# Kernel tuning notes

Hardware: AMD Instinct MI355X
Metric: run time of the kernel (lower is better)

Reference implementation:

```python
import jax, jax.numpy as jnp
import numpy as np

C1 = 512  # channels1 (query input dim)
C = 512   # channels (model dim)


def setup_inputs() -> dict:
    key = jax.random.key(0)
    ks = jax.random.split(key, 12)
    B, Lq, Lk = 8, 2048, 2048
    s1 = 1.0 / np.sqrt(C1)
    s = 1.0 / np.sqrt(C)
    return {
        "rep": jax.random.normal(ks[0], (B, Lq, C1), dtype=jnp.float32),
        "rep1": jax.random.normal(ks[1], (B, Lk, C), dtype=jnp.float32),
        "Wq_w": jax.random.uniform(ks[2], (C1, C), jnp.float32, -s1, s1),
        "Wq_b": jax.random.uniform(ks[3], (C,), jnp.float32, -s1, s1),
        "Wk_w": jax.random.uniform(ks[4], (C, C), jnp.float32, -s, s),
        "Wk_b": jax.random.uniform(ks[5], (C,), jnp.float32, -s, s),
        "Wv_w": jax.random.uniform(ks[6], (C, C), jnp.float32, -s, s),
        "Wv_b": jax.random.uniform(ks[7], (C,), jnp.float32, -s, s),
        "FC_w": jax.random.uniform(ks[8], (C, C), jnp.float32, -s, s),
        "FC_b": jax.random.uniform(ks[9], (C,), jnp.float32, -s, s),
    }


def reference(rep, rep1, Wq_w, Wq_b, Wk_w, Wk_b, Wv_w, Wv_b, FC_w, FC_b):
    # Linear + ReLU projections (single head)
    q = jax.nn.relu(jnp.einsum('blc,cd->bld', rep, Wq_w) + Wq_b)    # [B,Lq,C]
    k = jax.nn.relu(jnp.einsum('blc,cd->bld', rep1, Wk_w) + Wk_b)   # [B,Lk,C]
    v = jax.nn.relu(jnp.einsum('blc,cd->bld', rep1, Wv_w) + Wv_b)   # [B,Lk,C]
    scores = jnp.einsum('bqd,bkd->bqk', q, k) / jnp.sqrt(jnp.float32(C))
    attn = jax.nn.softmax(scores, axis=-1)                           # [B,Lq,Lk]
    out = jnp.einsum('bqk,bkd->bqd', attn, v)                        # [B,Lq,C]
    out = jax.nn.relu(jnp.einsum('bld,de->ble', out, FC_w) + FC_b)
    return out
```

## Files before the change

### kernel.cpp

```cpp
#include <hip/hip_runtime.h>


typedef __attribute__((ext_vector_type(8))) short short8;
typedef __attribute__((ext_vector_type(4))) float f32x4;

#define SEQ 2048
#define CH 512
#define NB 8
#define MTOT (NB * SEQ)

#define GLDS16(gp, lp)                                                                  \
  __builtin_amdgcn_global_load_lds((const __attribute__((address_space(1))) void*)(gp), \
                                   (__attribute__((address_space(3))) void*)(lp), 16, 0, 0)

__device__ __forceinline__ unsigned short f2bf(float f) {
  unsigned u = __float_as_uint(f);
  u += 0x7fffu + ((u >> 16) & 1u);
  return (unsigned short)(u >> 16);
}

__device__ __forceinline__ unsigned pack2bf(float lo, float hi) {
  return __builtin_amdgcn_perm(__float_as_uint(hi), __float_as_uint(lo), 0x07060302u);
}

__global__ __launch_bounds__(256) void prep2_kernel(
    const float* __restrict__ W0, const float* __restrict__ W1,
    const float* __restrict__ W2, const float* __restrict__ W3,
    unsigned short* __restrict__ Wt,
    const float* __restrict__ Wk_b, const float* __restrict__ Wv_b,
    float* __restrict__ biasKV, float* __restrict__ rowsum) {
  __shared__ __attribute__((aligned(16))) unsigned short tile[64 * 72];
  const int blk = blockIdx.x;
  const int t = threadIdx.x;
  if (blk < 256) {
    const int z = blk >> 6;
    const int bx = blk & 7, by = (blk >> 3) & 7;
    const float* W = (z == 0) ? W0 : (z == 1) ? W1 : (z == 2) ? W2 : W3;
    unsigned short* Wtz = Wt + (long)z * 512 * 512;
    const int k0 = by * 64, n0 = bx * 64;
    const int r = t >> 4, cq = (t & 15) * 4;
#pragma unroll
    for (int j = 0; j < 4; ++j) {
      int row = r + 16 * j;
      float4 v = *(const float4*)&W[(long)(k0 + row) * 512 + n0 + cq];
      tile[row * 72 + cq + 0] = f2bf(v.x);
      tile[row * 72 + cq + 1] = f2bf(v.y);
      tile[row * 72 + cq + 2] = f2bf(v.z);
      tile[row * 72 + cq + 3] = f2bf(v.w);
    }
    __syncthreads();
#pragma unroll
    for (int j = 0; j < 4; ++j) {
      int row = r + 16 * j;
      ushort4 o;
      o.x = tile[(cq + 0) * 72 + row];
      o.y = tile[(cq + 1) * 72 + row];
      o.z = tile[(cq + 2) * 72 + row];
      o.w = tile[(cq + 3) * 72 + row];
      *(ushort4*)&Wtz[(long)(n0 + row) * 512 + k0 + cq] = o;
    }
  } else if (blk == 256) {
    biasKV[t] = Wk_b[t];
    biasKV[t + 256] = Wk_b[t + 256];
    biasKV[t + 512] = Wv_b[t];
    biasKV[t + 768] = Wv_b[t + 256];
  } else {
    const int zb = blk - 257;
    f32x4 z4 = {0.f, 0.f, 0.f, 0.f};
    *(f32x4*)&rowsum[(zb * 256 + t) * 4] = z4;
  }
}

template <int LDO>
__device__ __forceinline__ void proj_body(const float* __restrict__ A,
                                          const unsigned short* __restrict__ Bt,
                                          const float* __restrict__ bias,
                                          unsigned short* __restrict__ Op,
                                          long m0, long n0, unsigned short* smem) {
  float* Af = (float*)smem;
  unsigned short* Bl = smem + 8192;
  const int t = threadIdx.x;
  const int w = t >> 6, l = t & 63;
  const int wr = w >> 1, wc = w & 1;
  const int lr = l & 15, lg = l >> 4;
  const float* ga = A + (m0 + 32 * w + (l >> 3)) * CH + ((l & 7) ^ (l >> 3)) * 4;
  const unsigned short* gb =
      Bt + (n0 + 32 * w + (l >> 2)) * CH + (((l & 3) ^ ((l >> 3) & 3)) * 8);
  float* la = Af + 32 * w * 32;
  unsigned short* lb = Bl + 32 * w * 32;

  f32x4 acc[4][4] = {};
  for (int k0 = 0; k0 < CH; k0 += 32) {
#pragma unroll
    for (int j = 0; j < 4; ++j) GLDS16(ga + 8 * j * CH, la + 8 * j * 32);
    GLDS16(gb, lb);
    GLDS16(gb + 16 * CH, lb + 16 * 32);
    ga += 32; gb += 32;
    __syncthreads();
    short8 af[4], bfr[4];
#pragma unroll
    for (int i = 0; i < 4; ++i) {
      const int row = 64 * wr + 16 * i + lr;
      f32x4 a0 = *(f32x4*)&Af[row * 32 + ((2 * lg) ^ (lr & 7)) * 4];
      f32x4 a1 = *(f32x4*)&Af[row * 32 + ((2 * lg + 1) ^ (lr & 7)) * 4];
      union { unsigned u[4]; short8 s; } pk;
      pk.u[0] = pack2bf(a0[0], a0[1]);
      pk.u[1] = pack2bf(a0[2], a0[3]);
      pk.u[2] = pack2bf(a1[0], a1[1]);
      pk.u[3] = pack2bf(a1[2], a1[3]);
      af[i] = pk.s;
      bfr[i] = *(short8*)&Bl[(64 * wc + 16 * i + lr) * 32 + (lg ^ ((lr >> 1) & 3)) * 8];
    }
#pragma unroll
    for (int mi = 0; mi < 4; ++mi)
#pragma unroll
      for (int ni = 0; ni < 4; ++ni)
        acc[mi][ni] =
            __builtin_amdgcn_mfma_f32_16x16x32_bf16(af[mi], bfr[ni], acc[mi][ni], 0, 0, 0);
    __syncthreads();
  }
  unsigned short* patch = smem;
  float bv[4];
#pragma unroll
  for (int ni = 0; ni < 4; ++ni) bv[ni] = bias[n0 + 64 * wc + 16 * ni + lr];
#pragma unroll
  for (int mi = 0; mi < 4; ++mi)
#pragma unroll
    for (int ni = 0; ni < 4; ++ni)
#pragma unroll
      for (int r = 0; r < 4; ++r) {
        const int m = 64 * wr + 16 * mi + 4 * lg + r;
        const int n = 64 * wc + 16 * ni + lr;
        patch[m * 128 + ((n >> 3) ^ (m & 15)) * 8 + (n & 7)] =
            f2bf(fmaxf(acc[mi][ni][r] + bv[ni], 0.0f));
      }
  __syncthreads();
  const int q = t & 3;
#pragma unroll
  for (int p = 0; p < 2; ++p) {
    const int m = 64 * p + (t >> 2);
#pragma unroll
    for (int i = 0; i < 4; ++i) {
      const int cc = i * 4 + q;
      short8 x = *(short8*)&patch[m * 128 + ((cc ^ (m & 15)) * 8)];
      *(short8*)&Op[(m0 + m) * LDO + n0 + cc * 8] = x;
    }
  }
}

__global__ __launch_bounds__(256) void proj_kernel(const float* __restrict__ rep,
                                                   const float* __restrict__ rep1,
                                                   const unsigned short* __restrict__ Wt,
                                                   const float* __restrict__ Wq_b,
                                                   const float* __restrict__ biasKV,
                                                   unsigned short* __restrict__ Qb,
                                                   unsigned short* __restrict__ KVb) {
  __shared__ __attribute__((aligned(16))) unsigned short smem[16384];
  const long m0 = (long)blockIdx.y * 128;
  if (blockIdx.x < 4)
    proj_body<CH>(rep, Wt, Wq_b, Qb, m0, (long)blockIdx.x * 128, smem);
  else
    proj_body<1024>(rep1, Wt + 512 * 512, biasKV, KVb, m0, (long)(blockIdx.x - 4) * 128, smem);
}

template <int EPI, int LDA, int LDB, int LDO, int K, int BK>
__device__ __forceinline__ void gemm_body(const unsigned short* __restrict__ A,
                                          const unsigned short* __restrict__ Bt,
                                          const float* __restrict__ bias,
                                          float* __restrict__ rowsum,
                                          void* __restrict__ outp,
                                          long m0, long n0, unsigned short* smem) {
  unsigned short* Al = smem;
  unsigned short* Bl = smem + 128 * BK;
  const int t = threadIdx.x;
  const int w = t >> 6, l = t & 63;
  const int wr = w >> 1, wc = w & 1;
  const int lr = l & 15, lg = l >> 4;
  constexpr int NC = BK / 8;
  const int rl = l / NC, cc0 = l % NC;
  unsigned short* la = &Al[32 * w * BK];
  unsigned short* lb = &Bl[32 * w * BK];
  const int srow = 32 * w + rl;
  const int sxor = (cc0 ^ (rl & (NC - 1))) * 8;
  const unsigned short* ga = A + (m0 + srow) * (long)LDA + sxor;
  const unsigned short* gb = Bt + (n0 + srow) * (long)LDB + sxor;

  f32x4 acc[4][4] = {};
  for (int k0 = 0; k0 < K; k0 += BK) {
#pragma unroll
    for (int j = 0; j < 4; ++j) {
      GLDS16(ga + (long)8 * j * LDA, la + j * 8 * BK);
      GLDS16(gb + (long)8 * j * LDB, lb + j * 8 * BK);
    }
    ga += BK; gb += BK;
    __syncthreads();
#pragma unroll
    for (int h = 0; h < BK / 32; ++h) {
      short8 af[4], bfr[4];
#pragma unroll
      for (int i = 0; i < 4; ++i) {
        const int kc = ((h * 4 + lg) ^ (lr & (NC - 1))) * 8;
        af[i]  = *(short8*)&Al[(64 * wr + 16 * i + lr) * BK + kc];
        bfr[i] = *(short8*)&Bl[(64 * wc + 16 * i + lr) * BK + kc];
      }
#pragma unroll
      for (int mi = 0; mi < 4; ++mi)
#pragma unroll
        for (int ni = 0; ni < 4; ++ni)
          acc[mi][ni] =
              __builtin_amdgcn_mfma_f32_16x16x32_bf16(af[mi], bfr[ni], acc[mi][ni], 0, 0, 0);
    }
    __syncthreads();
  }

  unsigned short* patch = smem;
  float rsum[4][4] = {};
#pragma unroll
  for (int mi = 0; mi < 4; ++mi)
#pragma unroll
    for (int ni = 0; ni < 4; ++ni)
#pragma unroll
      for (int r = 0; r < 4; ++r) {
        const int m = 64 * wr + 16 * mi + 4 * lg + r;
        const int n = 64 * wc + 16 * ni + lr;
        float a = acc[mi][ni][r];
        unsigned short ob;
        if (EPI == 6) ob = f2bf(a);
        else {
          float p = exp2f(a * 0.06375872f);
          ob = f2bf(p);
          rsum[mi][r] += __uint_as_float((unsigned)ob << 16);
        }
        patch[m * 128 + ((n >> 3) ^ (m & 15)) * 8 + (n & 7)] = ob;
      }
  __syncthreads();
  unsigned short* O = (unsigned short*)outp;
  const int q = t & 3;
#pragma unroll
  for (int p = 0; p < 2; ++p) {
    const int m = 64 * p + (t >> 2);
#pragma unroll
    for (int i = 0; i < 4; ++i) {
      const int cc = i * 4 + q;
      short8 x = *(short8*)&patch[m * 128 + ((cc ^ (m & 15)) * 8)];
      *(short8*)&O[(m0 + m) * LDO + n0 + cc * 8] = x;
    }
  }
  if (EPI == 2) {
#pragma unroll
    for (int off = 1; off < 16; off <<= 1)
#pragma unroll
      for (int mi = 0; mi < 4; ++mi)
#pragma unroll
        for (int r = 0; r < 4; ++r) rsum[mi][r] += __shfl_xor(rsum[mi][r], off);
    if (lr == 0) {
#pragma unroll
      for (int mi = 0; mi < 4; ++mi)
#pragma unroll
        for (int r = 0; r < 4; ++r)
          atomicAdd(&rowsum[m0 + 64 * wr + 16 * mi + 4 * lg + r], rsum[mi][r]);
    }
  }
}

__global__ __launch_bounds__(256) void qkvf_kernel(const unsigned short* __restrict__ Qb,
                                                   const unsigned short* __restrict__ KVb,
                                                   const unsigned short* __restrict__ WtF,
                                                   float* __restrict__ rowsum,
                                                   unsigned short* __restrict__ Pbuf,
                                                   unsigned short* __restrict__ VFt) {
  __shared__ __attribute__((aligned(16))) unsigned short smem[2 * 128 * 64];
  const int bz = blockIdx.z;
  if (blockIdx.y < 16) {
    gemm_body<2, CH, 1024, SEQ, CH, 64>(
        Qb + (long)bz * SEQ * CH, KVb + (long)bz * SEQ * 1024, nullptr,
        rowsum + (long)bz * SEQ, Pbuf + (long)bz * SEQ * SEQ,
        (long)blockIdx.y * 128, (long)blockIdx.x * 128, smem);
  } else {
    gemm_body<6, CH, 1024, SEQ, CH, 64>(
        WtF, KVb + 512 + (long)bz * SEQ * 1024, nullptr, nullptr,
        VFt + (long)bz * CH * SEQ,
        (long)(blockIdx.y - 16) * 128, (long)blockIdx.x * 128, smem);
  }
}

#define CFENCE asm volatile("" ::: "memory")
#define SB0 __builtin_amdgcn_sched_barrier(0)
#define BAR8                          \
  do {                                \
    CFENCE;                           \
    __builtin_amdgcn_s_barrier();     \
    SB0;                              \
  } while (0)
#define LGKM0                                            \
  do {                                                   \
    asm volatile("s_waitcnt lgkmcnt(0)" ::: "memory");   \
    SB0;                                                 \
  } while (0)
#define VMC(n)                                              \
  do {                                                      \
    asm volatile("s_waitcnt vmcnt(" #n ")" ::: "memory");   \
    SB0;                                                    \
  } while (0)

__global__ __launch_bounds__(512, 2) void pvf_kernel(const unsigned short* __restrict__ Pbuf,
                                                     const unsigned short* __restrict__ VFt,
                                                     const float* __restrict__ FC_b,
                                                     float* __restrict__ rowsum,
                                                     float* __restrict__ out) {
  __shared__ __attribute__((aligned(16))) unsigned short smem[3][24576];
  const int s = blockIdx.x;
  const int xcd = s & 7, j = s >> 3;
  const int x = j & 3, pg = j >> 2;
  const int y = xcd, bz = pg;
  const long m0 = (long)y * 256, n0 = (long)x * 128;

  const unsigned short* A  = Pbuf + (long)bz * SEQ * SEQ;
  const unsigned short* Bt = VFt + (long)bz * CH * SEQ;
  constexpr int LDA = SEQ, LDB = SEQ;
  constexpr int NT = SEQ / 64;

  const int t = threadIdx.x;
  const int w = t >> 6, l = t & 63;
  const int wr = w >> 1, wc = w & 1;
  const int lr = l & 15, lg = l >> 4;

  const int srow = t >> 3;
  const int schk = ((t & 7) ^ ((t >> 3) & 7)) * 8;
  const unsigned short* gA = A + (m0 + srow) * (long)LDA + schk;
  const unsigned short* gB = Bt + (n0 + srow) * (long)LDB + schk;

  auto stageA = [&](int c, int kt) {
#pragma unroll
    for (int jj = 0; jj < 4; ++jj) {
      unsigned short* d = &smem[c][(64 * jj + 8 * w) * 64];
      GLDS16(gA + (long)(64 * jj) * LDA + (long)kt * 64, d);
    }
  };
  auto stageB = [&](int c, int kt) {
#pragma unroll
    for (int jj = 0; jj < 2; ++jj) {
      unsigned short* d = &smem[c][16384 + (64 * jj + 8 * w) * 64];
      GLDS16(gB + (long)(64 * jj) * LDB + (long)kt * 64, d);
    }
  };

  const int kx0 = (lg ^ (lr & 7)) * 8;
  const int kx1 = ((4 + lg) ^ (lr & 7)) * 8;
  short8 af[8], bf0[4], bf1[4];
  f32x4 acc[4][4] = {};

  auto readA = [&](int c) {
#pragma unroll
    for (int i = 0; i < 4; ++i) {
      const unsigned short* p = &smem[c][(64 * wr + 16 * i + lr) * 64];
      af[2 * i]     = *(const short8*)&p[kx0];
      af[2 * i + 1] = *(const short8*)&p[kx1];
    }
  };
  auto readB = [&](int c, int nh, short8* bf) {
#pragma unroll
    for (int i = 0; i < 2; ++i) {
      const unsigned short* p = &smem[c][16384 + (64 * wc + 16 * (2 * nh + i) + lr) * 64];
      bf[2 * i]     = *(const short8*)&p[kx0];
      bf[2 * i + 1] = *(const short8*)&p[kx1];
    }
  };
  auto quad = [&](int nh, const short8* bf) {
    __builtin_amdgcn_s_setprio(1);
#pragma unroll
    for (int mi = 0; mi < 4; ++mi)
#pragma unroll
      for (int jj = 0; jj < 2; ++jj) {
        acc[mi][2 * nh + jj] = __builtin_amdgcn_mfma_f32_16x16x32_bf16(
            af[2 * mi], bf[2 * jj], acc[mi][2 * nh + jj], 0, 0, 0);
        acc[mi][2 * nh + jj] = __builtin_amdgcn_mfma_f32_16x16x32_bf16(
            af[2 * mi + 1], bf[2 * jj + 1], acc[mi][2 * nh + jj], 0, 0, 0);
      }
    __builtin_amdgcn_s_setprio(0);
  };

  stageA(0, 0); stageB(0, 0);
  stageA(1, 1); stageB(1, 1);
  VMC(6);
  BAR8;

#pragma unroll
  for (int kt = 0; kt < NT; ++kt) {
    const int b = kt % 3, nb = (kt + 2) % 3;
    const bool st = (kt + 2) < NT;
    readA(b); readB(b, 0, bf0);
    if (st) stageA(nb, kt + 2);
    BAR8; LGKM0; quad(0, bf0); BAR8;
    readB(b, 1, bf1);
    if (st) { stageB(nb, kt + 2); VMC(6); } else { VMC(0); }
    BAR8; LGKM0; quad(1, bf1); BAR8;
  }

  __syncthreads();
  float* patchF = (float*)&smem[0][0];
  float bv[4];
#pragma unroll
  for (int ni = 0; ni < 4; ++ni) bv[ni] = FC_b[n0 + 64 * wc + 16 * ni + lr];
  float inv[4][4];
#pragma unroll
  for (int mi = 0; mi < 4; ++mi)
#pragma unroll
    for (int r = 0; r < 4; ++r)
      inv[mi][r] = 1.0f / rowsum[(long)bz * SEQ + m0 + 64 * wr + 16 * mi + 4 * lg + r];
#pragma unroll
  for (int mi = 0; mi < 4; ++mi)
#pragma unroll
    for (int ni = 0; ni < 4; ++ni)
#pragma unroll
      for (int r = 0; r < 4; ++r) {
        const int m = 64 * wr + 16 * mi + 4 * lg + r;
        const int n = 64 * wc + 16 * ni + lr;
        patchF[m * 128 + ((n >> 2) ^ (m & 31)) * 4 + (n & 3)] =
            fmaxf(acc[mi][ni][r] * inv[mi][r] + bv[ni], 0.0f);
      }
  __syncthreads();
  {
    float* O = out + (long)bz * SEQ * CH;
    const int q = t & 3, mr = t >> 2;
#pragma unroll
    for (int p2 = 0; p2 < 2; ++p2) {
      const int m = 128 * p2 + mr;
#pragma unroll
      for (int i = 0; i < 8; ++i) {
        const int cc = i * 4 + q;
        f32x4 v = *(f32x4*)&patchF[m * 128 + ((cc ^ (m & 31)) * 4)];
        *(f32x4*)&O[(m0 + m) * CH + n0 + cc * 4] = v;
      }
    }
  }
}

extern "C" void kernel_launch(void* const* d_in, const int* in_sizes, int n_in,
                              void* d_out, int out_size, void* d_ws, size_t ws_size,
                              hipStream_t stream) {
  const float* rep  = (const float*)d_in[0];
  const float* rep1 = (const float*)d_in[1];
  const float* Wq_w = (const float*)d_in[2];
  const float* Wq_b = (const float*)d_in[3];
  const float* Wk_w = (const float*)d_in[4];
  const float* Wk_b = (const float*)d_in[5];
  const float* Wv_w = (const float*)d_in[6];
  const float* Wv_b = (const float*)d_in[7];
  const float* FC_w = (const float*)d_in[8];
  const float* FC_b = (const float*)d_in[9];
  float* out = (float*)d_out;
  char* ws = (char*)d_ws;

  const size_t MB = 1024 * 1024;
  unsigned short* Qb     = (unsigned short*)(ws + 0 * MB);
  unsigned short* KVb    = (unsigned short*)(ws + 16 * MB);
  unsigned short* VFt    = (unsigned short*)(ws + 48 * MB);
  unsigned short* Wt4    = (unsigned short*)(ws + 64 * MB);
  float*          biasKV = (float*)(ws + 66 * MB);
  unsigned short* Pbuf   = (unsigned short*)(ws + 67 * MB);
  float*          rowsum = (float*)(ws + 131 * MB);
  const size_t need = 132 * MB;
  if (ws_size < need) return;

  unsigned short* WtF = Wt4 + 3 * 512 * 512;

  prep2_kernel<<<273, 256, 0, stream>>>(Wq_w, Wk_w, Wv_w, FC_w, Wt4, Wk_b, Wv_b,
                                        biasKV, rowsum);

  proj_kernel<<<dim3(12, 128), 256, 0, stream>>>(rep, rep1, Wt4, Wq_b, biasKV, Qb, KVb);

  qkvf_kernel<<<dim3(16, 20, 8), 256, 0, stream>>>(Qb, KVb, WtF, rowsum, Pbuf, VFt);

  pvf_kernel<<<256, 512, 0, stream>>>(Pbuf, VFt, FC_b, rowsum, out);
}
```

Baseline: 291.6 us.

## Triple-buffer LDS loads in projection and QK/VF GEMMs with async prefetch

Replaces the single-buffered load-sync-compute loops in the projection kernel and the QK^T/VF GEMM with a three-stage LDS ring. Global-to-LDS loads run two K-tiles ahead, gated by explicit vmcnt waits and one barrier per step. The QK/VF GEMM also drops from a 64 to a 32 K-tile with a new swizzle to fit three buffers. This aims to hide global load latency behind MFMA work, at the cost of more LDS per block (72KB in proj), which may reduce occupancy.

```diff
diff --git a/kernel.cpp b/kernel.cpp
--- a/kernel.cpp
+++ b/kernel.cpp
@@ -22,6 +22,20 @@
 __device__ __forceinline__ unsigned pack2bf(float lo, float hi) {
   return __builtin_amdgcn_perm(__float_as_uint(hi), __float_as_uint(lo), 0x07060302u);
 }
+
+#define CFENCE asm volatile("" ::: "memory")
+#define SB0 __builtin_amdgcn_sched_barrier(0)
+#define BAR8                          \
+  do {                                \
+    CFENCE;                           \
+    __builtin_amdgcn_s_barrier();     \
+    SB0;                              \
+  } while (0)
+#define VMC(n)                                              \
+  do {                                                      \
+    asm volatile("s_waitcnt vmcnt(" #n ")" ::: "memory");   \
+    SB0;                                                    \
+  } while (0)
 
 __global__ __launch_bounds__(256) void prep2_kernel(
     const float* __restrict__ W0, const float* __restrict__ W1,
@@ -77,8 +91,6 @@
                                           const float* __restrict__ bias,
                                           unsigned short* __restrict__ Op,
                                           long m0, long n0, unsigned short* smem) {
-  float* Af = (float*)smem;
-  unsigned short* Bl = smem + 8192;
   const int t = threadIdx.x;
   const int w = t >> 6, l = t & 63;
   const int wr = w >> 1, wc = w & 1;
@@ -86,30 +98,41 @@
   const float* ga = A + (m0 + 32 * w + (l >> 3)) * CH + ((l & 7) ^ (l >> 3)) * 4;
   const unsigned short* gb =
       Bt + (n0 + 32 * w + (l >> 2)) * CH + (((l & 3) ^ ((l >> 3) & 3)) * 8);
-  float* la = Af + 32 * w * 32;
-  unsigned short* lb = Bl + 32 * w * 32;
+
+  auto stage = [&](int c, int kt) {
+    float* Ac = (float*)(smem + (long)c * 12288);
+    unsigned short* Bc = smem + (long)c * 12288 + 8192;
+#pragma unroll
+    for (int j = 0; j < 4; ++j)
+      GLDS16(ga + (long)8 * j * CH + kt * 32, Ac + (32 * w + 8 * j) * 32);
+    GLDS16(gb + kt * 32, Bc + 32 * w * 32);
+    GLDS16(gb + (long)16 * CH + kt * 32, Bc + (32 * w + 16) * 32);
+  };
 
   f32x4 acc[4][4] = {};
-  for (int k0 = 0; k0 < CH; k0 += 32) {
-#pragma unroll
-    for (int j = 0; j < 4; ++j) GLDS16(ga + 8 * j * CH, la + 8 * j * 32);
-    GLDS16(gb, lb);
-    GLDS16(gb + 16 * CH, lb + 16 * 32);
-    ga += 32; gb += 32;
-    __syncthreads();
+  constexpr int NT = CH / 32;
+  stage(0, 0); stage(1, 1);
+  VMC(6);
+  BAR8;
+#pragma unroll
+  for (int kt = 0; kt < NT; ++kt) {
+    const int c = kt % 3;
+    if (kt + 2 < NT) stage((kt + 2) % 3, kt + 2);
+    const float* Ac = (const float*)(smem + (long)c * 12288);
+    const unsigned short* Bc = smem + (long)c * 12288 + 8192;
     short8 af[4], bfr[4];
 #pragma unroll
     for (int i = 0; i < 4; ++i) {
       const int row = 64 * wr + 16 * i + lr;
-      f32x4 a0 = *(f32x4*)&Af[row * 32 + ((2 * lg) ^ (lr & 7)) * 4];
-      f32x4 a1 = *(f32x4*)&Af[row * 32 + ((2 * lg + 1) ^ (lr & 7)) * 4];
+      f32x4 a0 = *(f32x4*)&Ac[row * 32 + ((2 * lg) ^ (lr & 7)) * 4];
+      f32x4 a1 = *(f32x4*)&Ac[row * 32 + ((2 * lg + 1) ^ (lr & 7)) * 4];
       union { unsigned u[4]; short8 s; } pk;
       pk.u[0] = pack2bf(a0[0], a0[1]);
       pk.u[1] = pack2bf(a0[2], a0[3]);
       pk.u[2] = pack2bf(a1[0], a1[1]);
       pk.u[3] = pack2bf(a1[2], a1[3]);
       af[i] = pk.s;
-      bfr[i] = *(short8*)&Bl[(64 * wc + 16 * i + lr) * 32 + (lg ^ ((lr >> 1) & 3)) * 8];
+      bfr[i] = *(short8*)&Bc[(64 * wc + 16 * i + lr) * 32 + (lg ^ ((lr >> 1) & 3)) * 8];
     }
 #pragma unroll
     for (int mi = 0; mi < 4; ++mi)
@@ -117,7 +140,8 @@
       for (int ni = 0; ni < 4; ++ni)
         acc[mi][ni] =
             __builtin_amdgcn_mfma_f32_16x16x32_bf16(af[mi], bfr[ni], acc[mi][ni], 0, 0, 0);
-    __syncthreads();
+    if (kt + 2 < NT) { VMC(6); } else if (kt + 1 < NT) { VMC(0); }
+    BAR8;
   }
   unsigned short* patch = smem;
   float bv[4];
@@ -155,7 +179,7 @@
                                                    const float* __restrict__ biasKV,
                                                    unsigned short* __restrict__ Qb,
                                                    unsigned short* __restrict__ KVb) {
-  __shared__ __attribute__((aligned(16))) unsigned short smem[16384];
+  __shared__ __attribute__((aligned(16))) unsigned short smem[36864];
   const long m0 = (long)blockIdx.y * 128;
   if (blockIdx.x < 4)
     proj_body<CH>(rep, Wt, Wq_b, Qb, m0, (long)blockIdx.x * 128, smem);
@@ -163,54 +187,57 @@
     proj_body<1024>(rep1, Wt + 512 * 512, biasKV, KVb, m0, (long)(blockIdx.x - 4) * 128, smem);
 }
 
-template <int EPI, int LDA, int LDB, int LDO, int K, int BK>
-__device__ __forceinline__ void gemm_body(const unsigned short* __restrict__ A,
-                                          const unsigned short* __restrict__ Bt,
-                                          const float* __restrict__ bias,
-                                          float* __restrict__ rowsum,
-                                          void* __restrict__ outp,
-                                          long m0, long n0, unsigned short* smem) {
-  unsigned short* Al = smem;
-  unsigned short* Bl = smem + 128 * BK;
+template <int EPI, int LDA, int LDB, int LDO, int K>
+__device__ __forceinline__ void gemm_body32(const unsigned short* __restrict__ A,
+                                            const unsigned short* __restrict__ Bt,
+                                            float* __restrict__ rowsum,
+                                            void* __restrict__ outp,
+                                            long m0, long n0, unsigned short* smem) {
   const int t = threadIdx.x;
   const int w = t >> 6, l = t & 63;
   const int wr = w >> 1, wc = w & 1;
   const int lr = l & 15, lg = l >> 4;
-  constexpr int NC = BK / 8;
-  const int rl = l / NC, cc0 = l % NC;
-  unsigned short* la = &Al[32 * w * BK];
-  unsigned short* lb = &Bl[32 * w * BK];
-  const int srow = 32 * w + rl;
-  const int sxor = (cc0 ^ (rl & (NC - 1))) * 8;
-  const unsigned short* ga = A + (m0 + srow) * (long)LDA + sxor;
-  const unsigned short* gb = Bt + (n0 + srow) * (long)LDB + sxor;
+  const int srow = t >> 2;
+  const int sxor = ((t & 3) ^ (srow & 3)) * 8;
+  const unsigned short* gA = A + (m0 + srow) * (long)LDA + sxor;
+  const unsigned short* gB = Bt + (n0 + srow) * (long)LDB + sxor;
+
+  auto stage = [&](int c, int kt) {
+    unsigned short* Ac = smem + c * 8192;
+    unsigned short* Bc = Ac + 4096;
+#pragma unroll
+    for (int j = 0; j < 2; ++j) {
+      GLDS16(gA + (long)(64 * j) * LDA + kt * 32, Ac + (64 * j + 16 * w) * 32);
+      GLDS16(gB + (long)(64 * j) * LDB + kt * 32, Bc + (64 * j + 16 * w) * 32);
+    }
+  };
 
   f32x4 acc[4][4] = {};
-  for (int k0 = 0; k0 < K; k0 += BK) {
-#pragma unroll
-    for (int j = 0; j < 4; ++j) {
-      GLDS16(ga + (long)8 * j * LDA, la + j * 8 * BK);
-      GLDS16(gb + (long)8 * j * LDB, lb + j * 8 * BK);
-    }
-    ga += BK; gb += BK;
-    __syncthreads();
-#pragma unroll
-    for (int h = 0; h < BK / 32; ++h) {
-      short8 af[4], bfr[4];
-#pragma unroll
-      for (int i = 0; i < 4; ++i) {
-        const int kc = ((h * 4 + lg) ^ (lr & (NC - 1))) * 8;
-        af[i]  = *(short8*)&Al[(64 * wr + 16 * i + lr) * BK + kc];
-        bfr[i] = *(short8*)&Bl[(64 * wc + 16 * i + lr) * BK + kc];
-      }
-#pragma unroll
-      for (int mi = 0; mi < 4; ++mi)
-#pragma unroll
-        for (int ni = 0; ni < 4; ++ni)
-          acc[mi][ni] =
-              __builtin_amdgcn_mfma_f32_16x16x32_bf16(af[mi], bfr[ni], acc[mi][ni], 0, 0, 0);
-    }
-    __syncthreads();
+  constexpr int NT = K / 32;
+  stage(0, 0); stage(1, 1);
+  VMC(4);
+  BAR8;
+#pragma unroll
+  for (int kt = 0; kt < NT; ++kt) {
+    const int c = kt % 3;
+    if (kt + 2 < NT) stage((kt + 2) % 3, kt + 2);
+    const unsigned short* Ac = smem + c * 8192;
+    const unsigned short* Bc = Ac + 4096;
+    short8 af[4], bfr[4];
+    const int kc = (lg ^ (lr & 3)) * 8;
+#pragma unroll
+    for (int i = 0; i < 4; ++i) {
+      af[i]  = *(const short8*)&Ac[(64 * wr + 16 * i + lr) * 32 + kc];
+      bfr[i] = *(const short8*)&Bc[(64 * wc + 16 * i + lr) * 32 + kc];
+    }
+#pragma unroll
+    for (int mi = 0; mi < 4; ++mi)
+#pragma unroll
+      for (int ni = 0; ni < 4; ++ni)
+        acc[mi][ni] =
+            __builtin_amdgcn_mfma_f32_16x16x32_bf16(af[mi], bfr[ni], acc[mi][ni], 0, 0, 0);
+    if (kt + 2 < NT) { VMC(4); } else if (kt + 1 < NT) { VMC(0); }
+    BAR8;
   }
 
   unsigned short* patch = smem;
@@ -269,38 +296,25 @@
                                                    float* __restrict__ rowsum,
                                                    unsigned short* __restrict__ Pbuf,
                                                    unsigned short* __restrict__ VFt) {
-  __shared__ __attribute__((aligned(16))) unsigned short smem[2 * 128 * 64];
+  __shared__ __attribute__((aligned(16))) unsigned short smem[3 * 8192];
   const int bz = blockIdx.z;
   if (blockIdx.y < 16) {
-    gemm_body<2, CH, 1024, SEQ, CH, 64>(
-        Qb + (long)bz * SEQ * CH, KVb + (long)bz * SEQ * 1024, nullptr,
+    gemm_body32<2, CH, 1024, SEQ, CH>(
+        Qb + (long)bz * SEQ * CH, KVb + (long)bz * SEQ * 1024,
         rowsum + (long)bz * SEQ, Pbuf + (long)bz * SEQ * SEQ,
         (long)blockIdx.y * 128, (long)blockIdx.x * 128, smem);
   } else {
-    gemm_body<6, CH, 1024, SEQ, CH, 64>(
-        WtF, KVb + 512 + (long)bz * SEQ * 1024, nullptr, nullptr,
+    gemm_body32<6, CH, 1024, SEQ, CH>(
+        WtF, KVb + 512 + (long)bz * SEQ * 1024, nullptr,
         VFt + (long)bz * CH * SEQ,
         (long)(blockIdx.y - 16) * 128, (long)blockIdx.x * 128, smem);
   }
 }
 
-#define CFENCE asm volatile("" ::: "memory")
-#define SB0 __builtin_amdgcn_sched_barrier(0)
-#define BAR8                          \
-  do {                                \
-    CFENCE;                           \
-    __builtin_amdgcn_s_barrier();     \
-    SB0;                              \
-  } while (0)
 #define LGKM0                                            \
   do {                                                   \
     asm volatile("s_waitcnt lgkmcnt(0)" ::: "memory");   \
     SB0;                                                 \
-  } while (0)
-#define VMC(n)                                              \
-  do {                                                      \
-    asm volatile("s_waitcnt vmcnt(" #n ")" ::: "memory");   \
-    SB0;                                                    \
   } while (0)
 
 __global__ __launch_bounds__(512, 2) void pvf_kernel(const unsigned short* __restrict__ Pbuf,
```

New measurement: 285.1 us. -2.2%, faster.
